# Performance work log

Hardware: AMD Instinct MI355X
Metric: run time of the kernel (lower is better)

The kernel has to match this reference:

```python
import jax, jax.numpy as jnp
import numpy as np

B, C, H, W = 4, 256, 48, 48
HEADS, DIM_HEAD, SCALE = 8, 64, 10.0
INNER = HEADS * DIM_HEAD
EPS = 1e-12


def setup_inputs() -> dict:
    key = jax.random.key(0)
    k1, k2, k3, k4 = jax.random.split(key, 4)
    x = jax.random.normal(k1, (B, C, H, W), dtype=jnp.float32)
    # 1x1 conv weights stored as [out_ch, in_ch]
    w_qkv = jax.random.normal(k2, (3 * INNER, C), dtype=jnp.float32) * (1.0 / np.sqrt(C))
    w_out = jax.random.normal(k3, (C, INNER), dtype=jnp.float32) * (1.0 / np.sqrt(INNER))
    b_out = jax.random.normal(k4, (C,), dtype=jnp.float32) * 0.01
    return {"x": x, "w_qkv": w_qkv, "w_out": w_out, "b_out": b_out}


def _l2norm(t):
    # normalize along last axis, clamping the norm at EPS (matches torch l2norm)
    denom = jnp.maximum(jnp.linalg.norm(t, axis=-1, keepdims=True), EPS)
    return t / denom


def reference(x, w_qkv, w_out, b_out):
    b, c, h, w = x.shape
    n = h * w
    # 1x1 conv QKV projection: [B, 3*INNER, H, W]
    qkv = jnp.einsum('oc,bchw->bohw', w_qkv, x)
    q, k, v = jnp.split(qkv, 3, axis=1)
    # [B, heads, dim_head, N] -> [B, heads, N, dim_head]
    def to_bhnd(t):
        return t.reshape(b, HEADS, DIM_HEAD, n).transpose(0, 1, 3, 2)
    q = _l2norm(to_bhnd(q))
    k = _l2norm(to_bhnd(k))
    v = to_bhnd(v)
    sim = jnp.einsum('bhid,bhjd->bhij', q, k) * SCALE  # [B,h,N,N]
    attn = jax.nn.softmax(sim, axis=-1)
    out = jnp.einsum('bhij,bhjd->bhid', attn, v)  # [B,h,N,d]
    # back to [B, INNER, H, W]
    out = out.transpose(0, 1, 3, 2).reshape(b, INNER, h, w)
    # 1x1 conv output projection with bias
    out = jnp.einsum('oc,bchw->bohw', w_out, out) + b_out[None, :, None, None]
    return out
```

## Files before the change

kernel.cpp:

```cpp
#include <hip/hip_runtime.h>

typedef unsigned short u16;
typedef __attribute__((ext_vector_type(8))) short bf16x8;
typedef __attribute__((ext_vector_type(4))) float f32x4;
typedef __attribute__((ext_vector_type(16))) float f32x16;

#define MFMA16(A,B,C) __builtin_amdgcn_mfma_f32_16x16x32_bf16(A,B,C,0,0,0)
#define MFMA32(A,B,C) __builtin_amdgcn_mfma_f32_32x32x16_bf16(A,B,C,0,0,0)

#define B_ 4
#define C_ 256
#define N_ 2304
#define HEADS_ 8
#define DH_ 64
#define INNER_ 512
#define SCALE_LOG2E 14.426950408889634f

__device__ __forceinline__ u16 f2bf(float f) {
    union { float f; unsigned int u; } v; v.f = f;
    unsigned int r = v.u + 0x7fffu + ((v.u >> 16) & 1u);
    return (u16)(r >> 16);
}
__device__ __forceinline__ float bf2f(u16 h) {
    union { unsigned int u; float f; } v; v.u = ((unsigned int)h) << 16;
    return v.f;
}
__device__ __forceinline__ unsigned int cvtpk(float a, float b) {
    unsigned int r;
    asm("v_cvt_pk_bf16_f32 %0, %1, %2" : "=v"(r) : "v"(a), "v"(b));
    return r;
}
__device__ __forceinline__ void pl32swap(unsigned &a, unsigned &b) {
    asm volatile("v_permlane32_swap_b32 %0, %1" : "+v"(a), "+v"(b));
}
__device__ __forceinline__ float fexp2(float x) {
    float r;
    asm("v_exp_f32 %0, %1" : "=v"(r) : "v"(x));
    return r;
}

__global__ __launch_bounds__(256) void k_prep(const float* __restrict__ x,
                                              u16* __restrict__ xT,
                                              const float* __restrict__ w_qkv,
                                              u16* __restrict__ wqb,
                                              const float* __restrict__ w_out,
                                              u16* __restrict__ wob) {
    __shared__ float tile[64][65];
    int idx = blockIdx.x;
    int t = threadIdx.x;
    if (idx < 576) {
        int b = idx / 144, rem = idx % 144;
        int n0 = (rem >> 2) * 64, c0 = (rem & 3) * 64;
        const float* xb = x + (size_t)b * C_ * N_;
        u16* xTb = xT + (size_t)b * N_ * C_;
        int r = t >> 4;
        int q4 = (t & 15) * 4;
#pragma unroll
        for (int pass = 0; pass < 4; ++pass) {
            int c = r + pass * 16;
            float4 v = *(const float4*)(xb + (size_t)(c0 + c) * N_ + n0 + q4);
            tile[c][q4+0] = v.x; tile[c][q4+1] = v.y; tile[c][q4+2] = v.z; tile[c][q4+3] = v.w;
        }
        __syncthreads();
#pragma unroll
        for (int pass = 0; pass < 4; ++pass) {
            int n = r + pass * 16;
            ushort4 o;
            o.x = f2bf(tile[q4+0][n]); o.y = f2bf(tile[q4+1][n]);
            o.z = f2bf(tile[q4+2][n]); o.w = f2bf(tile[q4+3][n]);
            *(ushort4*)(xTb + (size_t)(n0 + n) * C_ + c0 + q4) = o;
        }
    } else if (idx < 960) {
        int i = (idx - 576) * 256 + t;
        float4 v = ((const float4*)w_qkv)[i];
        ushort4 o;
        o.x = f2bf(v.x); o.y = f2bf(v.y); o.z = f2bf(v.z); o.w = f2bf(v.w);
        ((ushort4*)wqb)[i] = o;
    } else {
        int i = (idx - 960) * 256 + t;
        float4 v = ((const float4*)w_out)[i];
        ushort4 o;
        o.x = f2bf(v.x); o.y = f2bf(v.y); o.z = f2bf(v.z); o.w = f2bf(v.w);
        ((ushort4*)wob)[i] = o;
    }
}

__global__ __launch_bounds__(256) void k_qkv(const u16* __restrict__ w_qkv,
                                             const u16* __restrict__ xT,
                                             u16* __restrict__ Qn,
                                             u16* __restrict__ Kn,
                                             u16* __restrict__ Vt) {
    __shared__ __align__(16) u16 Wt[64][264];
    __shared__ __align__(16) u16 Xt[64][264];
    int mt = blockIdx.x, nt = blockIdx.y, b = blockIdx.z;
    int tid = threadIdx.x;
    int wv = tid >> 6, lane = tid & 63;
    int col = lane & 15, quad = lane >> 4;
    int o0 = mt * 64;
    const u16* wtile = w_qkv + (size_t)o0 * C_;
    const u16* xtile = xT + ((size_t)b * N_ + nt*64) * C_;
#pragma unroll
    for (int p = 0; p < 8; ++p) {
        int c = p * 256 + tid;
        int row = c >> 5, seg = c & 31;
        *(uint4*)(&Wt[row][seg*8]) = *(const uint4*)(wtile + (size_t)row * C_ + seg*8);
        *(uint4*)(&Xt[row][seg*8]) = *(const uint4*)(xtile + (size_t)row * C_ + seg*8);
    }
    __syncthreads();
    f32x4 z = {0.f, 0.f, 0.f, 0.f};
    f32x4 acc[4]; acc[0]=z; acc[1]=z; acc[2]=z; acc[3]=z;
#pragma unroll
    for (int ks = 0; ks < 8; ++ks) {
        bf16x8 bfrag = *(const bf16x8*)(&Xt[wv*16 + col][ks*32 + quad*8]);
#pragma unroll
        for (int mb = 0; mb < 4; ++mb) {
            bf16x8 afrag = *(const bf16x8*)(&Wt[mb*16 + col][ks*32 + quad*8]);
            acc[mb] = MFMA16(afrag, bfrag, acc[mb]);
        }
    }
    int n = nt * 64 + wv * 16 + col;
    int which = mt >> 3, h = mt & 7;
    if (which < 2) {
        float s = 0.f;
#pragma unroll
        for (int mb = 0; mb < 4; ++mb)
#pragma unroll
            for (int r = 0; r < 4; ++r) s += acc[mb][r] * acc[mb][r];
        s += __shfl_xor(s, 16);
        s += __shfl_xor(s, 32);
        float inv = 1.f / fmaxf(sqrtf(s), 1e-12f);
        if (which == 0) inv *= SCALE_LOG2E;
        u16* dst = (which == 0 ? Qn : Kn) + (((size_t)b * HEADS_ + h) * N_ + n) * DH_;
#pragma unroll
        for (int mb = 0; mb < 4; ++mb) {
            uint2 o;
            o.x = cvtpk(acc[mb][0] * inv, acc[mb][1] * inv);
            o.y = cvtpk(acc[mb][2] * inv, acc[mb][3] * inv);
            *(uint2*)(dst + mb*16 + quad*4) = o;
        }
    } else {
        u16* dst = Vt + ((size_t)b * HEADS_ + h) * (size_t)DH_ * N_;
#pragma unroll
        for (int mb = 0; mb < 4; ++mb)
#pragma unroll
            for (int r = 0; r < 4; ++r)
                dst[(size_t)(mb*16 + quad*4 + r) * N_ + n] = f2bf(acc[mb][r]);
    }
}

__device__ __forceinline__ void store_o32(const f32x16 O, u16* dst, int hi) {
    unsigned c0 = cvtpk(O[0], O[1]),  c1 = cvtpk(O[2], O[3]);
    unsigned c2 = cvtpk(O[4], O[5]),  c3 = cvtpk(O[6], O[7]);
    unsigned c4 = cvtpk(O[8], O[9]),  c5 = cvtpk(O[10], O[11]);
    unsigned c6 = cvtpk(O[12], O[13]), c7 = cvtpk(O[14], O[15]);
    pl32swap(c0, c2); pl32swap(c1, c3);
    pl32swap(c4, c6); pl32swap(c5, c7);
    uint4 w0; w0.x = c0; w0.y = c1; w0.z = c2; w0.w = c3;
    uint4 w1; w1.x = c4; w1.y = c5; w1.z = c6; w1.w = c7;
    *(uint4*)(dst + hi*8)      = w0;
    *(uint4*)(dst + 16 + hi*8) = w1;
}

__global__ __launch_bounds__(256) void k_attn_split(const u16* __restrict__ Qn,
                                                    const u16* __restrict__ Kn,
                                                    const u16* __restrict__ Vt,
                                                    u16* __restrict__ Opb,
                                                    float* __restrict__ lp) {
    __shared__ __align__(16) u16 Kt[64][72];
    __shared__ __align__(16) u16 Vtl[64][72];
    int head_lin = blockIdx.x & 31;
    int rest = blockIdx.x >> 5;
    int qt = rest % 18;
    int ksplit = rest / 18;
    int b = head_lin >> 3, h = head_lin & 7;
    int tid = threadIdx.x;
    int wv = tid >> 6, lane = tid & 63;
    int q32 = lane & 31, hi = lane >> 5;
    size_t head = (size_t)b * HEADS_ + h;
    const u16* Qh = Qn + head * (size_t)N_ * DH_;
    const u16* Kh = Kn + head * (size_t)N_ * DH_ + (size_t)ksplit * 576 * DH_;
    const u16* Vh = Vt + head * (size_t)DH_ * N_;
    int q0 = qt * 128 + wv * 32;
    bf16x8 qf[4];
#pragma unroll
    for (int ds = 0; ds < 4; ++ds)
        qf[ds] = *(const bf16x8*)(Qh + (size_t)(q0 + q32) * DH_ + ds*16 + hi*8);
    f32x16 accO0, accO1;
#pragma unroll
    for (int i = 0; i < 16; ++i) { accO0[i] = 0.f; accO1[i] = 0.f; }
    float lsum = 0.f;
    int srow = tid >> 3, sseg = tid & 7;
    const u16* ksrc0 = Kh + (size_t)tid * 8;
    const u16* vsrc0 = Vh + (size_t)srow * N_ + ksplit * 576 + sseg * 8;

    uint4 k0 = *(const uint4*)(ksrc0);
    uint4 k1 = *(const uint4*)(ksrc0 + 2048);
    uint4 v0 = *(const uint4*)(vsrc0);
    uint4 v1 = *(const uint4*)(vsrc0 + (size_t)32 * N_);

    for (int kt = 0; kt < 9; ++kt) {
        *(uint4*)(&Kt[srow][sseg*8])      = k0;
        *(uint4*)(&Kt[32 + srow][sseg*8]) = k1;
        *(uint4*)(&Vtl[srow][sseg*8])      = v0;
        *(uint4*)(&Vtl[32 + srow][sseg*8]) = v1;
        __syncthreads();
        int ktn = kt + 1 < 9 ? kt + 1 : kt;
        k0 = *(const uint4*)(ksrc0 + (size_t)ktn * 4096);
        k1 = *(const uint4*)(ksrc0 + (size_t)ktn * 4096 + 2048);
        v0 = *(const uint4*)(vsrc0 + ktn * 64);
        v1 = *(const uint4*)(vsrc0 + (size_t)32 * N_ + ktn * 64);
#pragma unroll
        for (int kb = 0; kb < 2; ++kb) {
            f32x16 s;
#pragma unroll
            for (int i = 0; i < 16; ++i) s[i] = 0.f;
#pragma unroll
            for (int ds = 0; ds < 4; ++ds) {
                bf16x8 kf = *(const bf16x8*)(&Kt[kb*32 + q32][ds*16 + hi*8]);
                s = MFMA32(kf, qf[ds], s);
            }
#pragma unroll
            for (int i = 0; i < 16; ++i) s[i] = fexp2(s[i]);
            lsum += ( ((s[0]+s[1])+(s[2]+s[3])) + ((s[4]+s[5])+(s[6]+s[7])) )
                  + ( ((s[8]+s[9])+(s[10]+s[11])) + ((s[12]+s[13])+(s[14]+s[15])) );
            unsigned c0 = cvtpk(s[0], s[1]),  c1 = cvtpk(s[2], s[3]);
            unsigned c2 = cvtpk(s[4], s[5]),  c3 = cvtpk(s[6], s[7]);
            unsigned c4 = cvtpk(s[8], s[9]),  c5 = cvtpk(s[10], s[11]);
            unsigned c6 = cvtpk(s[12], s[13]), c7 = cvtpk(s[14], s[15]);
            pl32swap(c0, c2); pl32swap(c1, c3);
            pl32swap(c4, c6); pl32swap(c5, c7);
            union { unsigned u[4]; bf16x8 v; } pf0, pf1;
            pf0.u[0] = c0; pf0.u[1] = c1; pf0.u[2] = c2; pf0.u[3] = c3;
            pf1.u[0] = c4; pf1.u[1] = c5; pf1.u[2] = c6; pf1.u[3] = c7;
            bf16x8 vf00 = *(const bf16x8*)(&Vtl[q32][kb*32 + hi*8]);
            bf16x8 vf01 = *(const bf16x8*)(&Vtl[32 + q32][kb*32 + hi*8]);
            accO0 = MFMA32(vf00, pf0.v, accO0);
            accO1 = MFMA32(vf01, pf0.v, accO1);
            bf16x8 vf10 = *(const bf16x8*)(&Vtl[q32][kb*32 + 16 + hi*8]);
            bf16x8 vf11 = *(const bf16x8*)(&Vtl[32 + q32][kb*32 + 16 + hi*8]);
            accO0 = MFMA32(vf10, pf1.v, accO0);
            accO1 = MFMA32(vf11, pf1.v, accO1);
        }
        __syncthreads();
    }
    lsum += __shfl_xor(lsum, 32);
    u16* dst = Opb + (((size_t)ksplit * B_ + b) * N_ + q0 + q32) * INNER_ + h * DH_;
    store_o32(accO0, dst, hi);
    store_o32(accO1, dst + 32, hi);
    if (hi == 0) {
        size_t lbase = (((size_t)ksplit * B_ + b) * HEADS_ + h) * N_;
        lp[lbase + q0 + q32] = lsum;
    }
}

__global__ __launch_bounds__(256) void k_comb(const u16* __restrict__ Opb,
                                              const float* __restrict__ lp,
                                              u16* __restrict__ AO) {
    int g = blockIdx.x * 256 + threadIdx.x;
    int b = g / 294912;
    int rem = g % 294912;
    int n = rem >> 7;
    int i4 = rem & 127;
    int h = i4 >> 4;
    float s0 = 0.f, s1 = 0.f, s2 = 0.f, s3 = 0.f, l = 0.f;
#pragma unroll
    for (int s = 0; s < 4; ++s) {
        ushort4 p = ((const ushort4*)Opb)[g + (size_t)s * 1179648];
        s0 += bf2f(p.x); s1 += bf2f(p.y); s2 += bf2f(p.z); s3 += bf2f(p.w);
        l += lp[(((size_t)s * B_ + b) * HEADS_ + h) * N_ + n];
    }
    float inv = 1.f / l;
    uint2 o;
    o.x = cvtpk(s0 * inv, s1 * inv);
    o.y = cvtpk(s2 * inv, s3 * inv);
    ((uint2*)AO)[g] = o;
}

__global__ __launch_bounds__(256) void k_attn(const u16* __restrict__ Qn,
                                              const u16* __restrict__ Kn,
                                              const u16* __restrict__ Vt,
                                              u16* __restrict__ AO) {
    __shared__ __align__(16) u16 Kt[64][72];
    __shared__ __align__(16) u16 Vtl[64][72];
    __shared__ __align__(16) u16 plds[4][32][72];
    int head_lin = blockIdx.x & 31;
    int qt = blockIdx.x >> 5;
    int b = head_lin >> 3, h = head_lin & 7;
    int tid = threadIdx.x;
    int wv = tid >> 6, lane = tid & 63;
    int col = lane & 15, quad = lane >> 4;
    size_t head = (size_t)b * HEADS_ + h;
    const u16* Qh = Qn + head * (size_t)N_ * DH_;
    const u16* Kh = Kn + head * (size_t)N_ * DH_;
    const u16* Vh = Vt + head * (size_t)DH_ * N_;
    int q0 = qt * 128 + wv * 32;
    bf16x8 qfA0 = *(const bf16x8*)(Qh + (size_t)(q0 + col) * DH_ + quad*8);
    bf16x8 qfA1 = *(const bf16x8*)(Qh + (size_t)(q0 + col) * DH_ + 32 + quad*8);
    bf16x8 qfB0 = *(const bf16x8*)(Qh + (size_t)(q0 + 16 + col) * DH_ + quad*8);
    bf16x8 qfB1 = *(const bf16x8*)(Qh + (size_t)(q0 + 16 + col) * DH_ + 32 + quad*8);
    f32x4 z = {0.f, 0.f, 0.f, 0.f};
    f32x4 OA[4], OB[4];
#pragma unroll
    for (int i = 0; i < 4; ++i) { OA[i] = z; OB[i] = z; }
    float lA = 0.f, lB = 0.f;
    int srow = tid >> 3, sseg = tid & 7;
    const u16* ksrc0 = Kh + (size_t)tid * 8;
    const u16* vsrc0 = Vh + (size_t)srow * N_ + sseg * 8;
    uint4 k0 = *(const uint4*)(ksrc0);
    uint4 k1 = *(const uint4*)(ksrc0 + 2048);
    uint4 v0 = *(const uint4*)(vsrc0);
    uint4 v1 = *(const uint4*)(vsrc0 + (size_t)32 * N_);
    for (int kt = 0; kt < N_/64; ++kt) {
        *(uint4*)(&Kt[srow][sseg*8])      = k0;
        *(uint4*)(&Kt[32 + srow][sseg*8]) = k1;
        *(uint4*)(&Vtl[srow][sseg*8])      = v0;
        *(uint4*)(&Vtl[32 + srow][sseg*8]) = v1;
        __syncthreads();
        int ktn = kt + 1 < N_/64 ? kt + 1 : kt;
        k0 = *(const uint4*)(ksrc0 + (size_t)ktn * 4096);
        k1 = *(const uint4*)(ksrc0 + (size_t)ktn * 4096 + 2048);
        v0 = *(const uint4*)(vsrc0 + ktn * 64);
        v1 = *(const uint4*)(vsrc0 + (size_t)32 * N_ + ktn * 64);
        float rsA = 0.f, rsB = 0.f;
#pragma unroll
        for (int nb = 0; nb < 4; ++nb) {
            bf16x8 kf0 = *(const bf16x8*)(&Kt[nb*16 + col][quad*8]);
            bf16x8 kf1 = *(const bf16x8*)(&Kt[nb*16 + col][32 + quad*8]);
            f32x4 a = MFMA16(kf0, qfA0, z);
            a = MFMA16(kf1, qfA1, a);
            f32x4 c = MFMA16(kf0, qfB0, z);
            c = MFMA16(kf1, qfB1, c);
            float a0 = fexp2(a[0]);
            float a1 = fexp2(a[1]);
            float a2 = fexp2(a[2]);
            float a3 = fexp2(a[3]);
            float c0 = fexp2(c[0]);
            float c1 = fexp2(c[1]);
            float c2 = fexp2(c[2]);
            float c3 = fexp2(c[3]);
            rsA += (a0 + a1) + (a2 + a3);
            rsB += (c0 + c1) + (c2 + c3);
            uint2 wA, wB;
            wA.x = cvtpk(a0, a1); wA.y = cvtpk(a2, a3);
            wB.x = cvtpk(c0, c1); wB.y = cvtpk(c2, c3);
            *(uint2*)(&plds[wv][col][nb*16 + quad*4]) = wA;
            *(uint2*)(&plds[wv][16 + col][nb*16 + quad*4]) = wB;
        }
        lA += rsA; lB += rsB;
        __asm__ volatile("" ::: "memory");
#pragma unroll
        for (int ks = 0; ks < 2; ++ks) {
            bf16x8 pfA = *(const bf16x8*)(&plds[wv][col][ks*32 + quad*8]);
            bf16x8 pfB = *(const bf16x8*)(&plds[wv][16 + col][ks*32 + quad*8]);
#pragma unroll
            for (int nb = 0; nb < 4; ++nb) {
                bf16x8 vf = *(const bf16x8*)(&Vtl[nb*16 + col][ks*32 + quad*8]);
                OA[nb] = MFMA16(vf, pfA, OA[nb]);
                OB[nb] = MFMA16(vf, pfB, OB[nb]);
            }
        }
        __asm__ volatile("" ::: "memory");
        __syncthreads();
    }
    lA += __shfl_xor(lA, 16); lA += __shfl_xor(lA, 32);
    lB += __shfl_xor(lB, 16); lB += __shfl_xor(lB, 32);
    float linvA = 1.f / lA, linvB = 1.f / lB;
    u16* dstA = AO + ((size_t)b * N_ + q0 + col) * INNER_ + h * DH_;
    u16* dstB = AO + ((size_t)b * N_ + q0 + 16 + col) * INNER_ + h * DH_;
#pragma unroll
    for (int nb = 0; nb < 4; ++nb) {
        uint2 wA, wB;
        wA.x = cvtpk(OA[nb][0] * linvA, OA[nb][1] * linvA);
        wA.y = cvtpk(OA[nb][2] * linvA, OA[nb][3] * linvA);
        wB.x = cvtpk(OB[nb][0] * linvB, OB[nb][1] * linvB);
        wB.y = cvtpk(OB[nb][2] * linvB, OB[nb][3] * linvB);
        *(uint2*)(dstA + nb*16 + quad*4) = wA;
        *(uint2*)(dstB + nb*16 + quad*4) = wB;
    }
}

__global__ __launch_bounds__(256) void k_proj(const u16* __restrict__ w_out,
                                              const float* __restrict__ b_out,
                                              const u16* __restrict__ AO,
                                              float* __restrict__ out) {
    __shared__ __align__(16) u16 Wt[64][264];
    __shared__ __align__(16) u16 At[64][264];
    int mt = blockIdx.x, nt = blockIdx.y, b = blockIdx.z;
    int tid = threadIdx.x;
    int wv = tid >> 6, lane = tid & 63;
    int col = lane & 15, quad = lane >> 4;
    int o0b = mt * 64;
    const u16* wtile = w_out + (size_t)o0b * INNER_;
    const u16* atile = AO + ((size_t)b * N_ + nt*64) * INNER_;
    f32x4 z = {0.f, 0.f, 0.f, 0.f};
    f32x4 acc[4]; acc[0]=z; acc[1]=z; acc[2]=z; acc[3]=z;
#pragma unroll
    for (int half = 0; half < 2; ++half) {
        if (half) __syncthreads();
#pragma unroll
        for (int p = 0; p < 8; ++p) {
            int c = p * 256 + tid;
            int row = c >> 5, seg = c & 31;
            *(uint4*)(&Wt[row][seg*8]) =
                *(const uint4*)(wtile + (size_t)row * INNER_ + half*256 + seg*8);
            *(uint4*)(&At[row][seg*8]) =
                *(const uint4*)(atile + (size_t)row * INNER_ + half*256 + seg*8);
        }
        __syncthreads();
#pragma unroll
        for (int ks = 0; ks < 8; ++ks) {
            bf16x8 af = *(const bf16x8*)(&Wt[wv*16 + col][ks*32 + quad*8]);
#pragma unroll
            for (int nb = 0; nb < 4; ++nb) {
                bf16x8 bfv = *(const bf16x8*)(&At[nb*16 + col][ks*32 + quad*8]);
                acc[nb] = MFMA16(af, bfv, acc[nb]);
            }
        }
    }
    int o0 = o0b + wv * 16;
    float bias[4];
#pragma unroll
    for (int r = 0; r < 4; ++r) bias[r] = b_out[o0 + quad*4 + r];
    float* dst = out + ((size_t)b * C_ + o0) * N_ + nt*64;
#pragma unroll
    for (int nb = 0; nb < 4; ++nb)
#pragma unroll
        for (int r = 0; r < 4; ++r)
            dst[(size_t)(quad*4 + r) * N_ + nb*16 + col] = acc[nb][r] + bias[r];
}

extern "C" void kernel_launch(void* const* d_in, const int* in_sizes, int n_in,
                              void* d_out, int out_size, void* d_ws, size_t ws_size,
                              hipStream_t stream) {
    const float* x     = (const float*)d_in[0];
    const float* w_qkv = (const float*)d_in[1];
    const float* w_out = (const float*)d_in[2];
    const float* b_out = (const float*)d_in[3];
    float* out = (float*)d_out;

    char* ws = (char*)d_ws;
    u16* xT  = (u16*)(ws);
    u16* Qn  = (u16*)(ws + 4718592);
    u16* Kn  = (u16*)(ws + 14155776);
    u16* Vt  = (u16*)(ws + 23592960);
    u16* AO  = (u16*)(ws + 33030144);
    u16* wqb = (u16*)(ws + 42467328);
    u16* wob = (u16*)(ws + 43253760);
    u16* Opb = (u16*)(ws + 43515904);
    float* lp = (float*)(ws + 1179648);
    const size_t need = 81854464;

    hipLaunchKernelGGL(k_prep, dim3(1088), dim3(256), 0, stream, x, xT, w_qkv, wqb, w_out, wob);
    hipLaunchKernelGGL(k_qkv,  dim3(24, N_/64, B_), dim3(256), 0, stream, wqb, xT, Qn, Kn, Vt);
    if (ws_size >= need) {
        hipLaunchKernelGGL(k_attn_split, dim3(2304), dim3(256), 0, stream, Qn, Kn, Vt, Opb, lp);
        hipLaunchKernelGGL(k_comb, dim3(4608), dim3(256), 0, stream, Opb, lp, AO);
    } else {
        hipLaunchKernelGGL(k_attn, dim3((N_/128) * 32), dim3(256), 0, stream, Qn, Kn, Vt, AO);
    }
    hipLaunchKernelGGL(k_proj, dim3(C_/64, N_/64, B_), dim3(256), 0, stream, wob, b_out, AO, out);
}
```

Before: 166.4 us.

## Double-buffer K/V tiles in LDS and interleave QK with softmax/PV under setprio

Makes the K/V shared-memory tiles double-buffered, so each iteration needs one barrier instead of two and the next tile is written to the alternate buffer after compute. Both QK score blocks are issued up front, and the exp/pack of one block is interleaved with the PV MFMAs of the other. s_setprio raises wave priority around the MFMA phases to encourage overlap across waves. LDS use doubles and register pressure rises from holding two score blocks at once.

```diff
diff --git a/kernel.cpp b/kernel.cpp
--- a/kernel.cpp
+++ b/kernel.cpp
@@ -161,13 +161,29 @@
     *(uint4*)(dst + 16 + hi*8) = w1;
 }
 
+#define SM_PACK(S, PF0, PF1, LSUM)                                              \
+    {                                                                           \
+        _Pragma("unroll")                                                       \
+        for (int i = 0; i < 16; ++i) S[i] = fexp2(S[i]);                        \
+        LSUM += ( ((S[0]+S[1])+(S[2]+S[3])) + ((S[4]+S[5])+(S[6]+S[7])) )       \
+              + ( ((S[8]+S[9])+(S[10]+S[11])) + ((S[12]+S[13])+(S[14]+S[15])) );\
+        unsigned c0 = cvtpk(S[0], S[1]),  c1 = cvtpk(S[2], S[3]);               \
+        unsigned c2 = cvtpk(S[4], S[5]),  c3 = cvtpk(S[6], S[7]);               \
+        unsigned c4 = cvtpk(S[8], S[9]),  c5 = cvtpk(S[10], S[11]);             \
+        unsigned c6 = cvtpk(S[12], S[13]), c7 = cvtpk(S[14], S[15]);            \
+        pl32swap(c0, c2); pl32swap(c1, c3);                                     \
+        pl32swap(c4, c6); pl32swap(c5, c7);                                     \
+        PF0.u[0] = c0; PF0.u[1] = c1; PF0.u[2] = c2; PF0.u[3] = c3;             \
+        PF1.u[0] = c4; PF1.u[1] = c5; PF1.u[2] = c6; PF1.u[3] = c7;             \
+    }
+
 __global__ __launch_bounds__(256) void k_attn_split(const u16* __restrict__ Qn,
                                                     const u16* __restrict__ Kn,
                                                     const u16* __restrict__ Vt,
                                                     u16* __restrict__ Opb,
                                                     float* __restrict__ lp) {
-    __shared__ __align__(16) u16 Kt[64][72];
-    __shared__ __align__(16) u16 Vtl[64][72];
+    __shared__ __align__(16) u16 Kt[2][64][72];
+    __shared__ __align__(16) u16 Vtl[2][64][72];
     int head_lin = blockIdx.x & 31;
     int rest = blockIdx.x >> 5;
     int qt = rest % 18;
@@ -197,51 +213,72 @@
     uint4 k1 = *(const uint4*)(ksrc0 + 2048);
     uint4 v0 = *(const uint4*)(vsrc0);
     uint4 v1 = *(const uint4*)(vsrc0 + (size_t)32 * N_);
+    *(uint4*)(&Kt[0][srow][sseg*8])       = k0;
+    *(uint4*)(&Kt[0][32 + srow][sseg*8])  = k1;
+    *(uint4*)(&Vtl[0][srow][sseg*8])      = v0;
+    *(uint4*)(&Vtl[0][32 + srow][sseg*8]) = v1;
+    int cur = 0;
 
     for (int kt = 0; kt < 9; ++kt) {
-        *(uint4*)(&Kt[srow][sseg*8])      = k0;
-        *(uint4*)(&Kt[32 + srow][sseg*8]) = k1;
-        *(uint4*)(&Vtl[srow][sseg*8])      = v0;
-        *(uint4*)(&Vtl[32 + srow][sseg*8]) = v1;
         __syncthreads();
         int ktn = kt + 1 < 9 ? kt + 1 : kt;
         k0 = *(const uint4*)(ksrc0 + (size_t)ktn * 4096);
         k1 = *(const uint4*)(ksrc0 + (size_t)ktn * 4096 + 2048);
         v0 = *(const uint4*)(vsrc0 + ktn * 64);
         v1 = *(const uint4*)(vsrc0 + (size_t)32 * N_ + ktn * 64);
-#pragma unroll
-        for (int kb = 0; kb < 2; ++kb) {
-            f32x16 s;
-#pragma unroll
-            for (int i = 0; i < 16; ++i) s[i] = 0.f;
-#pragma unroll
-            for (int ds = 0; ds < 4; ++ds) {
-                bf16x8 kf = *(const bf16x8*)(&Kt[kb*32 + q32][ds*16 + hi*8]);
-                s = MFMA32(kf, qf[ds], s);
-            }
-#pragma unroll
-            for (int i = 0; i < 16; ++i) s[i] = fexp2(s[i]);
-            lsum += ( ((s[0]+s[1])+(s[2]+s[3])) + ((s[4]+s[5])+(s[6]+s[7])) )
-                  + ( ((s[8]+s[9])+(s[10]+s[11])) + ((s[12]+s[13])+(s[14]+s[15])) );
-            unsigned c0 = cvtpk(s[0], s[1]),  c1 = cvtpk(s[2], s[3]);
-            unsigned c2 = cvtpk(s[4], s[5]),  c3 = cvtpk(s[6], s[7]);
-            unsigned c4 = cvtpk(s[8], s[9]),  c5 = cvtpk(s[10], s[11]);
-            unsigned c6 = cvtpk(s[12], s[13]), c7 = cvtpk(s[14], s[15]);
-            pl32swap(c0, c2); pl32swap(c1, c3);
-            pl32swap(c4, c6); pl32swap(c5, c7);
-            union { unsigned u[4]; bf16x8 v; } pf0, pf1;
-            pf0.u[0] = c0; pf0.u[1] = c1; pf0.u[2] = c2; pf0.u[3] = c3;
-            pf1.u[0] = c4; pf1.u[1] = c5; pf1.u[2] = c6; pf1.u[3] = c7;
-            bf16x8 vf00 = *(const bf16x8*)(&Vtl[q32][kb*32 + hi*8]);
-            bf16x8 vf01 = *(const bf16x8*)(&Vtl[32 + q32][kb*32 + hi*8]);
-            accO0 = MFMA32(vf00, pf0.v, accO0);
-            accO1 = MFMA32(vf01, pf0.v, accO1);
-            bf16x8 vf10 = *(const bf16x8*)(&Vtl[q32][kb*32 + 16 + hi*8]);
-            bf16x8 vf11 = *(const bf16x8*)(&Vtl[32 + q32][kb*32 + 16 + hi*8]);
-            accO0 = MFMA32(vf10, pf1.v, accO0);
-            accO1 = MFMA32(vf11, pf1.v, accO1);
-        }
-        __syncthreads();
+        const u16 (*Ktc)[72]  = Kt[cur];
+        const u16 (*Vtc)[72]  = Vtl[cur];
+        f32x16 s0, s1;
+#pragma unroll
+        for (int i = 0; i < 16; ++i) { s0[i] = 0.f; s1[i] = 0.f; }
+        __builtin_amdgcn_s_setprio(1);
+#pragma unroll
+        for (int ds = 0; ds < 4; ++ds) {
+            bf16x8 kf = *(const bf16x8*)(&Ktc[q32][ds*16 + hi*8]);
+            s0 = MFMA32(kf, qf[ds], s0);
+        }
+#pragma unroll
+        for (int ds = 0; ds < 4; ++ds) {
+            bf16x8 kf = *(const bf16x8*)(&Ktc[32 + q32][ds*16 + hi*8]);
+            s1 = MFMA32(kf, qf[ds], s1);
+        }
+        __builtin_amdgcn_s_setprio(0);
+        union { unsigned u[4]; bf16x8 v; } pfA, pfB, pfC, pfD;
+        SM_PACK(s0, pfA, pfB, lsum)
+        __builtin_amdgcn_s_setprio(1);
+        {
+            bf16x8 vf00 = *(const bf16x8*)(&Vtc[q32][hi*8]);
+            bf16x8 vf01 = *(const bf16x8*)(&Vtc[32 + q32][hi*8]);
+            accO0 = MFMA32(vf00, pfA.v, accO0);
+            accO1 = MFMA32(vf01, pfA.v, accO1);
+            bf16x8 vf10 = *(const bf16x8*)(&Vtc[q32][16 + hi*8]);
+            bf16x8 vf11 = *(const bf16x8*)(&Vtc[32 + q32][16 + hi*8]);
+            accO0 = MFMA32(vf10, pfB.v, accO0);
+            accO1 = MFMA32(vf11, pfB.v, accO1);
+        }
+        __builtin_amdgcn_s_setprio(0);
+        SM_PACK(s1, pfC, pfD, lsum)
+        __builtin_amdgcn_s_setprio(1);
+        {
+            bf16x8 vf00 = *(const bf16x8*)(&Vtc[q32][32 + hi*8]);
+            bf16x8 vf01 = *(const bf16x8*)(&Vtc[32 + q32][32 + hi*8]);
+            accO0 = MFMA32(vf00, pfC.v, accO0);
+            accO1 = MFMA32(vf01, pfC.v, accO1);
+            bf16x8 vf10 = *(const bf16x8*)(&Vtc[q32][48 + hi*8]);
+            bf16x8 vf11 = *(const bf16x8*)(&Vtc[32 + q32][48 + hi*8]);
+            accO0 = MFMA32(vf10, pfD.v, accO0);
+            accO1 = MFMA32(vf11, pfD.v, accO1);
+        }
+        __builtin_amdgcn_s_setprio(0);
+        {
+            u16 (*Ktn_)[72] = Kt[cur ^ 1];
+            u16 (*Vtn_)[72] = Vtl[cur ^ 1];
+            *(uint4*)(&Ktn_[srow][sseg*8])      = k0;
+            *(uint4*)(&Ktn_[32 + srow][sseg*8]) = k1;
+            *(uint4*)(&Vtn_[srow][sseg*8])      = v0;
+            *(uint4*)(&Vtn_[32 + srow][sseg*8]) = v1;
+        }
+        cur ^= 1;
     }
     lsum += __shfl_xor(lsum, 32);
     u16* dst = Opb + (((size_t)ksplit * B_ + b) * N_ + q0 + q32) * INNER_ + h * DH_;
```

Measured after the change: 167.0 us. Within noise of the previous version (+0.4%).
